# Optimization experiments

Measured on AMD Instinct MI355X. Metric: run time of the kernel, lower is better.

The kernel has to match this reference:

```python
import jax, jax.numpy as jnp
import numpy as np

SIGMA_DIS = 3.0
MAX_LABELS = 33  # label ids in [0, 32]; 0 = background, 1..32 = kernels


def setup_inputs() -> dict:
    key = jax.random.key(0)
    k1, k2 = jax.random.split(key)
    B, C, H, W = 8, 4, 896, 896
    pred = jax.random.normal(k1, (B, C, H, W), dtype=jnp.float32)
    kernels_mask = jnp.ones((B, H, W), dtype=jnp.float32)
    labels = jax.random.randint(k2, (B, H, W), 0, MAX_LABELS, dtype=jnp.int32)
    return {
        "pred_similarities": pred,
        "kernels_mask": kernels_mask,
        "kernel_mask_ndi_labels": labels,
    }


def _disc_loss(pred, labels, sigma):
    # pred: [B, C, H, W], labels: [B, H, W] int
    B, C = pred.shape[0], pred.shape[1]
    p = pred.reshape(B, C, -1)        # [B, C, N]
    lab = labels.reshape(B, -1)       # [B, N]

    # Masks for distinct labels are disjoint, so for a = pred*mask_i/|K_i|,
    # b = pred*mask_j/|K_j|:  ||a - b||_F^2 = s_i + s_j where
    # s_k = sum_{pixels in K_k} sum_c pred^2 / |K_k|^2.
    sq = jnp.sum(p * p, axis=1)       # [B, N]

    def seg(x, l):
        return jax.ops.segment_sum(x, l, num_segments=MAX_LABELS)

    card = jax.vmap(seg)(jnp.ones_like(sq), lab)   # [B, L] pixel counts
    ssq = jax.vmap(seg)(sq, lab)                   # [B, L] sum of squares
    safe_card = jnp.where(card > 0, card, 1.0)
    s = ssq / (safe_card * safe_card)              # [B, L]

    nk = jnp.max(lab, axis=1)                      # [B] num_kernels per image
    ks = jnp.arange(MAX_LABELS)
    valid = (ks[None, :] >= 1) & (ks[None, :] <= nk[:, None]) & (card > 0)  # [B, L]

    # all unordered pairs i < j of valid labels
    pair_mask = (
        valid[:, :, None] & valid[:, None, :] & (ks[:, None] < ks[None, :])[None]
    )  # [B, L, L]
    S = s[:, :, None] + s[:, None, :]
    S_safe = jnp.where(pair_mask, S, 1.0)          # keep sqrt grads finite
    # NOTE: original torch.max(norm, 0)[0] on a 0-d tensor is a dim-reduction
    # over a size-1 view and is an identity, NOT a clamp; replicated faithfully.
    d = sigma - jnp.sqrt(S_safe)
    term = jnp.log(d * d + 1.0)
    per_b = jnp.sum(jnp.where(pair_mask, term, 0.0), axis=(1, 2))  # [B]

    nk_f = nk.astype(per_b.dtype)
    denom = jnp.where(nk > 1, nk_f * (nk_f - 1.0), 1.0)
    loss_b = jnp.where(nk > 1, per_b / denom, 0.0)
    return jnp.sum(loss_b)


def reference(pred_similarities, kernels_mask, kernel_mask_ndi_labels):
    # kernels_mask is reshaped but never used by the original forward math.
    return _disc_loss(pred_similarities, kernel_mask_ndi_labels, SIGMA_DIS)
```

## Files before the change

### kernel.cpp

```cpp
#include <hip/hip_runtime.h>

#define MAXL 33
#define HSTRIDE 35
#define PB 128
#define TPB 128

__global__ __launch_bounds__(TPB, 2) void seg_hist_kernel(
    const float* __restrict__ pred, const int* __restrict__ labels,
    float* __restrict__ partial, int N) {
  const int b = blockIdx.y;
  const int ng = N >> 2;
  __shared__ unsigned long long hist[TPB * HSTRIDE];
  __shared__ float xred[2][2][MAXL];
  const int tid = threadIdx.x;

  unsigned long long* hp = &hist[tid * HSTRIDE];
#pragma unroll
  for (int i = 0; i < MAXL; ++i) hp[i] = 0ull;

  const float4* p = reinterpret_cast<const float4*>(pred) + (size_t)b * 4 * ng;
  const int4* lb = reinterpret_cast<const int4*>(labels) + (size_t)b * ng;

  for (int g = blockIdx.x * TPB + tid; g < ng; g += PB * TPB) {
    float4 c0 = p[g];
    float4 c1 = p[g + ng];
    float4 c2 = p[g + 2 * ng];
    float4 c3 = p[g + 3 * ng];
    int4 l = lb[g];
    float s0 = c0.x * c0.x + c1.x * c1.x + c2.x * c2.x + c3.x * c3.x;
    float s1 = c0.y * c0.y + c1.y * c1.y + c2.y * c2.y + c3.y * c3.y;
    float s2 = c0.z * c0.z + c1.z * c1.z + c2.z * c2.z + c3.z * c3.z;
    float s3 = c0.w * c0.w + c1.w * c1.w + c2.w * c2.w + c3.w * c3.w;

    unsigned long long v;
    v = hp[l.x];
    hp[l.x] = ((v >> 32) + 1ull) << 32 |
              (unsigned)__float_as_uint(__uint_as_float((unsigned)v) + s0);
    v = hp[l.y];
    hp[l.y] = ((v >> 32) + 1ull) << 32 |
              (unsigned)__float_as_uint(__uint_as_float((unsigned)v) + s1);
    v = hp[l.z];
    hp[l.z] = ((v >> 32) + 1ull) << 32 |
              (unsigned)__float_as_uint(__uint_as_float((unsigned)v) + s2);
    v = hp[l.w];
    hp[l.w] = ((v >> 32) + 1ull) << 32 |
              (unsigned)__float_as_uint(__uint_as_float((unsigned)v) + s3);
  }
  __syncthreads();

  const int wave = tid >> 6;
  const int lane = tid & 63;
  if (lane < MAXL) {
    float fs = 0.f;
    unsigned fc = 0u;
    for (int u = 0; u < 64; ++u) {
      unsigned long long v = hist[(wave * 64 + u) * HSTRIDE + lane];
      fs += __uint_as_float((unsigned)v);
      fc += (unsigned)(v >> 32);
    }
    xred[wave][0][lane] = fs;
    xred[wave][1][lane] = (float)fc;
  }
  __syncthreads();
  if (tid < MAXL) {
    float ssq = xred[0][0][tid] + xred[1][0][tid];
    float cnt = xred[0][1][tid] + xred[1][1][tid];
    partial[(size_t)(b * 2 * MAXL + tid) * PB + blockIdx.x] = ssq;
    partial[(size_t)(b * 2 * MAXL + MAXL + tid) * PB + blockIdx.x] = cnt;
  }
}

__global__ __launch_bounds__(512) void reduce_finalize_kernel(
    const float* __restrict__ partial, float* __restrict__ out) {
  __shared__ float red[8 * 2 * MAXL];
  __shared__ float s_val[8 * MAXL];
  __shared__ float s_flag[8 * MAXL];
  __shared__ float s_invden[8];
  __shared__ float s_part[8];
  const int tid = threadIdx.x;
  const int wave = tid >> 6;
  const int lane = tid & 63;

  const float2* src = reinterpret_cast<const float2*>(partial);
  for (int s0 = wave * 8; s0 < 8 * 2 * MAXL; s0 += 64) {
    float2 v[8];
#pragma unroll
    for (int u = 0; u < 8; ++u) v[u] = src[(size_t)(s0 + u) * (PB / 2) + lane];
#pragma unroll
    for (int u = 0; u < 8; ++u) {
      float t = v[u].x + v[u].y;
      for (int off = 32; off; off >>= 1) t += __shfl_down(t, off, 64);
      if (lane == 0) red[s0 + u] = t;
    }
  }
  __syncthreads();

  for (int i = tid; i < 8 * MAXL; i += 512) {
    int b = i / MAXL, l = i - b * MAXL;
    float cnt = red[b * 2 * MAXL + MAXL + l];
    float ssq = red[b * 2 * MAXL + l];
    float safe = cnt > 0.f ? cnt : 1.f;
    s_val[i] = ssq / (safe * safe);
    s_flag[i] = (l >= 1 && cnt > 0.f) ? 1.f : 0.f;
  }
  __syncthreads();
  if (tid < 8) {
    int nk = 0;
    for (int l = MAXL - 1; l >= 0; --l) {
      if (red[tid * 2 * MAXL + MAXL + l] > 0.f) {
        nk = l;
        break;
      }
    }
    s_invden[tid] = (nk > 1) ? 1.f / ((float)nk * ((float)nk - 1.f)) : 0.f;
  }
  __syncthreads();

  float local = 0.f;
  const int total = 8 * MAXL * MAXL;
  for (int idx = tid; idx < total; idx += 512) {
    int b = idx / (MAXL * MAXL);
    int r = idx - b * MAXL * MAXL;
    int i = r / MAXL;
    int j = r - i * MAXL;
    if (i < j && s_flag[b * MAXL + i] != 0.f && s_flag[b * MAXL + j] != 0.f) {
      float S = s_val[b * MAXL + i] + s_val[b * MAXL + j];
      float d = 3.0f - sqrtf(S);
      local += logf(d * d + 1.f) * s_invden[b];
    }
  }
  for (int off = 32; off; off >>= 1) local += __shfl_down(local, off, 64);
  if (lane == 0) s_part[wave] = local;
  __syncthreads();
  if (tid == 0) {
    float tot = 0.f;
    for (int w = 0; w < 8; ++w) tot += s_part[w];
    out[0] = tot;
  }
}

extern "C" void kernel_launch(void* const* d_in, const int* in_sizes, int n_in,
                              void* d_out, int out_size, void* d_ws,
                              size_t ws_size, hipStream_t stream) {
  const float* pred = (const float*)d_in[0];
  const int* labels = (const int*)d_in[2];
  float* out = (float*)d_out;

  const int B = 8;
  const int N = in_sizes[2] / B;

  float* partial = (float*)d_ws;

  dim3 grid(PB, B);
  seg_hist_kernel<<<grid, dim3(TPB), 0, stream>>>(pred, labels, partial, N);
  reduce_finalize_kernel<<<dim3(1), dim3(512), 0, stream>>>(partial, out);
}
```

Measured before the change: 48.41 us.

## Split packed LDS histogram, merge duplicate labels, prefetch next tile

Replaces the packed 64-bit sum/count shared-memory histogram with separate float and uint arrays. Within each group of four pixels, duplicate labels are merged so that independent LDS reads and writes can be issued without read-after-write hazards. The next iteration's global loads are software-prefetched into registers. The finalize kernel switches to a per-thread row reduction using float4 loads instead of per-wave shuffle reductions. The risks are more register use and LDS bank conflicts from the MAXL=33 stride.

```diff
diff --git a/kernel.cpp b/kernel.cpp
--- a/kernel.cpp
+++ b/kernel.cpp
@@ -1,7 +1,6 @@
 #include <hip/hip_runtime.h>
 
 #define MAXL 33
-#define HSTRIDE 35
 #define PB 128
 #define TPB 128
 
@@ -10,41 +9,73 @@
     float* __restrict__ partial, int N) {
   const int b = blockIdx.y;
   const int ng = N >> 2;
-  __shared__ unsigned long long hist[TPB * HSTRIDE];
+  __shared__ float sumh[TPB * MAXL];
+  __shared__ unsigned cnth[TPB * MAXL];
   __shared__ float xred[2][2][MAXL];
   const int tid = threadIdx.x;
 
-  unsigned long long* hp = &hist[tid * HSTRIDE];
+  float* sh = &sumh[tid * MAXL];
+  unsigned* ch = &cnth[tid * MAXL];
 #pragma unroll
-  for (int i = 0; i < MAXL; ++i) hp[i] = 0ull;
+  for (int i = 0; i < MAXL; ++i) {
+    sh[i] = 0.f;
+    ch[i] = 0u;
+  }
 
   const float4* p = reinterpret_cast<const float4*>(pred) + (size_t)b * 4 * ng;
   const int4* lb = reinterpret_cast<const int4*>(labels) + (size_t)b * ng;
-
-  for (int g = blockIdx.x * TPB + tid; g < ng; g += PB * TPB) {
-    float4 c0 = p[g];
-    float4 c1 = p[g + ng];
-    float4 c2 = p[g + 2 * ng];
-    float4 c3 = p[g + 3 * ng];
-    int4 l = lb[g];
+  const int STRIDE = PB * TPB;
+
+  int g = blockIdx.x * TPB + tid;
+  float4 c0 = p[g], c1 = p[g + ng], c2 = p[g + 2 * ng], c3 = p[g + 3 * ng];
+  int4 l = lb[g];
+
+  while (true) {
+    const int gn = g + STRIDE;
+    const bool more = gn < ng;
+    float4 n0, n1, n2, n3;
+    int4 nl;
+    if (more) {
+      n0 = p[gn];
+      n1 = p[gn + ng];
+      n2 = p[gn + 2 * ng];
+      n3 = p[gn + 3 * ng];
+      nl = lb[gn];
+    }
+
     float s0 = c0.x * c0.x + c1.x * c1.x + c2.x * c2.x + c3.x * c3.x;
     float s1 = c0.y * c0.y + c1.y * c1.y + c2.y * c2.y + c3.y * c3.y;
     float s2 = c0.z * c0.z + c1.z * c1.z + c2.z * c2.z + c3.z * c3.z;
     float s3 = c0.w * c0.w + c1.w * c1.w + c2.w * c2.w + c3.w * c3.w;
 
-    unsigned long long v;
-    v = hp[l.x];
-    hp[l.x] = ((v >> 32) + 1ull) << 32 |
-              (unsigned)__float_as_uint(__uint_as_float((unsigned)v) + s0);
-    v = hp[l.y];
-    hp[l.y] = ((v >> 32) + 1ull) << 32 |
-              (unsigned)__float_as_uint(__uint_as_float((unsigned)v) + s1);
-    v = hp[l.z];
-    hp[l.z] = ((v >> 32) + 1ull) << 32 |
-              (unsigned)__float_as_uint(__uint_as_float((unsigned)v) + s2);
-    v = hp[l.w];
-    hp[l.w] = ((v >> 32) + 1ull) << 32 |
-              (unsigned)__float_as_uint(__uint_as_float((unsigned)v) + s3);
+    const bool e01 = l.x == l.y, e02 = l.x == l.z, e03 = l.x == l.w;
+    const bool e12 = l.y == l.z, e13 = l.y == l.w, e23 = l.z == l.w;
+    const float w1 = s1 + (e01 ? s0 : 0.f);
+    const float w2 = s2 + (e12 ? s1 : 0.f) + (e02 ? s0 : 0.f);
+    const float w3 =
+        s3 + (e23 ? s2 : 0.f) + (e13 ? s1 : 0.f) + (e03 ? s0 : 0.f);
+    const unsigned m1 = 1u + (unsigned)e01;
+    const unsigned m2 = 1u + (unsigned)e12 + (unsigned)e02;
+    const unsigned m3 = 1u + (unsigned)e23 + (unsigned)e13 + (unsigned)e03;
+
+    const float r0 = sh[l.x], r1 = sh[l.y], r2 = sh[l.z], r3 = sh[l.w];
+    const unsigned q0 = ch[l.x], q1 = ch[l.y], q2 = ch[l.z], q3 = ch[l.w];
+    sh[l.x] = r0 + s0;
+    sh[l.y] = r1 + w1;
+    sh[l.z] = r2 + w2;
+    sh[l.w] = r3 + w3;
+    ch[l.x] = q0 + 1u;
+    ch[l.y] = q1 + m1;
+    ch[l.z] = q2 + m2;
+    ch[l.w] = q3 + m3;
+
+    if (!more) break;
+    c0 = n0;
+    c1 = n1;
+    c2 = n2;
+    c3 = n3;
+    l = nl;
+    g = gn;
   }
   __syncthreads();
 
@@ -53,20 +84,20 @@
   if (lane < MAXL) {
     float fs = 0.f;
     unsigned fc = 0u;
+#pragma unroll 8
     for (int u = 0; u < 64; ++u) {
-      unsigned long long v = hist[(wave * 64 + u) * HSTRIDE + lane];
-      fs += __uint_as_float((unsigned)v);
-      fc += (unsigned)(v >> 32);
+      fs += sumh[(wave * 64 + u) * MAXL + lane];
+      fc += cnth[(wave * 64 + u) * MAXL + lane];
     }
     xred[wave][0][lane] = fs;
     xred[wave][1][lane] = (float)fc;
   }
   __syncthreads();
   if (tid < MAXL) {
-    float ssq = xred[0][0][tid] + xred[1][0][tid];
-    float cnt = xred[0][1][tid] + xred[1][1][tid];
-    partial[(size_t)(b * 2 * MAXL + tid) * PB + blockIdx.x] = ssq;
-    partial[(size_t)(b * 2 * MAXL + MAXL + tid) * PB + blockIdx.x] = cnt;
+    partial[(size_t)(b * 2 * MAXL + tid) * PB + blockIdx.x] =
+        xred[0][0][tid] + xred[1][0][tid];
+    partial[(size_t)(b * 2 * MAXL + MAXL + tid) * PB + blockIdx.x] =
+        xred[0][1][tid] + xred[1][1][tid];
   }
 }
 
@@ -81,17 +112,31 @@
   const int wave = tid >> 6;
   const int lane = tid & 63;
 
-  const float2* src = reinterpret_cast<const float2*>(partial);
-  for (int s0 = wave * 8; s0 < 8 * 2 * MAXL; s0 += 64) {
-    float2 v[8];
-#pragma unroll
-    for (int u = 0; u < 8; ++u) v[u] = src[(size_t)(s0 + u) * (PB / 2) + lane];
-#pragma unroll
-    for (int u = 0; u < 8; ++u) {
-      float t = v[u].x + v[u].y;
-      for (int off = 32; off; off >>= 1) t += __shfl_down(t, off, 64);
-      if (lane == 0) red[s0 + u] = t;
-    }
+  {
+    int slot = tid;
+    const float4* row =
+        reinterpret_cast<const float4*>(partial) + (size_t)slot * (PB / 4);
+    float a0 = 0.f, a1 = 0.f;
+#pragma unroll 8
+    for (int u = 0; u < PB / 4; u += 2) {
+      float4 x = row[u], y = row[u + 1];
+      a0 += x.x + x.y + x.z + x.w;
+      a1 += y.x + y.y + y.z + y.w;
+    }
+    if (slot < 8 * 2 * MAXL) red[slot] = a0 + a1;
+  }
+  if (tid < 8 * 2 * MAXL - 512) {
+    int slot = 512 + tid;
+    const float4* row =
+        reinterpret_cast<const float4*>(partial) + (size_t)slot * (PB / 4);
+    float a0 = 0.f, a1 = 0.f;
+#pragma unroll 8
+    for (int u = 0; u < PB / 4; u += 2) {
+      float4 x = row[u], y = row[u + 1];
+      a0 += x.x + x.y + x.z + x.w;
+      a1 += y.x + y.y + y.z + y.w;
+    }
+    red[slot] = a0 + a1;
   }
   __syncthreads();
 
```

Result: faster. 39.45 us (median of 2 runs) (-18.5%).
